# Kernel optimization log

Measured on AMD Instinct MI355X. Metric: run time of the kernel, lower is better.

The kernel has to match this reference:

```python
import jax, jax.numpy as jnp
import numpy as np

N_EDGE_TYPES = 25
EF = 2  # edge feature dim (excluding type)
HID = 10


def _edge_nn(et, ef, emb, wh, bh, wg, bg):
    # y = relu(emb[et] * (ef@Wh+bh) + (ef@Wg+bg)) -> [E, in*out]
    return jax.nn.relu(emb[et] * (ef @ wh + bh) + (ef @ wg + bg))


def _nnconv(x, et, ef, src, dst, emb, wh, bh, wg, bg, root, bias, in_c, out_c):
    n = x.shape[0]
    w = _edge_nn(et, ef, emb, wh, bh, wg, bg).reshape(-1, in_c, out_c)  # [E,in,out]
    msg = jnp.einsum('ei,eio->eo', x[src], w)                          # per-edge matmul
    s = jax.ops.segment_sum(msg, dst, num_segments=n)
    cnt = jax.ops.segment_sum(jnp.ones((src.shape[0],), x.dtype), dst, num_segments=n)
    agg = s / jnp.maximum(cnt, 1.0)[:, None]                           # scatter-mean
    return agg + x @ root + bias


def _make_params(key, in_c, out_c):
    ks = jax.random.split(key, 6)
    d = in_c * out_c
    s = 0.1
    return dict(
        emb=jax.random.normal(ks[0], (N_EDGE_TYPES, d), jnp.float32) * s,
        wh=jax.random.normal(ks[1], (EF, d), jnp.float32) * s,
        bh=jax.random.normal(ks[2], (d,), jnp.float32) * s,
        wg=jax.random.normal(ks[3], (EF, d), jnp.float32) * s,
        bg=jax.random.normal(ks[4], (d,), jnp.float32) * s,
        root=jax.random.normal(ks[5], (in_c, out_c), jnp.float32) * s,
        bias=jnp.zeros((out_c,), jnp.float32),
    )


def setup_inputs() -> dict:
    key = jax.random.key(0)
    ks = jax.random.split(key, 12)
    N, E, IN_C, OUT_C, B = 50000, 250000, 16, 16, 8
    inp = {
        'x': jax.random.normal(ks[0], (N, IN_C), jnp.float32),
        'edge_feat': jax.random.normal(ks[1], (E, EF), jnp.float32),
        'edge_type': jax.random.randint(ks[2], (E,), 0, N_EDGE_TYPES),
        'edge_src': jax.random.randint(ks[3], (E,), 0, N),
        'edge_dst': jax.random.randint(ks[4], (E,), 0, N),
        'cell_type': jax.random.randint(ks[5], (N,), 0, 3),
        'batch_ids': jnp.sort(jax.random.randint(ks[6], (N,), 0, B)),
        'batch_size': B,
    }
    for i, (ic, oc) in enumerate([(IN_C, HID), (HID, HID), (HID, OUT_C)], start=1):
        p = _make_params(ks[6 + i], ic, oc)
        for k, v in p.items():
            inp[f'{k}{i}'] = v
    return inp


def reference(x, edge_feat,
              emb1, wh1, bh1, wg1, bg1, root1, bias1,
              emb2, wh2, bh2, wg2, bg2, root2, bias2,
              emb3, wh3, bh3, wg3, bg3, root3, bias3,
              edge_type, edge_src, edge_dst, cell_type, batch_ids, batch_size):
    in_c, out_c = x.shape[1], root3.shape[1]
    h = _nnconv(x, edge_type, edge_feat, edge_src, edge_dst,
                emb1, wh1, bh1, wg1, bg1, root1, bias1, in_c, HID)
    h = jax.nn.relu(h)  # dropout is identity in eval mode
    h = _nnconv(h, edge_type, edge_feat, edge_src, edge_dst,
                emb2, wh2, bh2, wg2, bg2, root2, bias2, HID, HID)
    h = jax.nn.relu(h)
    h = _nnconv(h, edge_type, edge_feat, edge_src, edge_dst,
                emb3, wh3, bh3, wg3, bg3, root3, bias3, HID, out_c)
    h = jax.nn.relu(h)
    # scatter-mean pooling over nodes with cell_type==1, grouped by graph id
    gate = (cell_type == 1).astype(jnp.int32)
    idx = gate * (batch_ids.astype(jnp.int32) + 1)  # 0 = discarded bucket
    nseg = batch_size + 1
    s = jax.ops.segment_sum(h, idx, num_segments=nseg)
    cnt = jax.ops.segment_sum(jnp.ones((h.shape[0],), h.dtype), idx, num_segments=nseg)
    pooled = s / jnp.maximum(cnt, 1.0)[:, None]
    return pooled[1:batch_size + 1, :]  # [B, out_c]
```

## Files before the change

### kernel.cpp

```cpp
#include <hip/hip_runtime.h>
#include <stdint.h>

#define IN1 16
#define HIDC 10
#define OUT3 16
#define NTYPES 25
#define MAXB 8
#define HSTR 12

#define D1 (IN1 * HIDC)
#define D2 (HIDC * HIDC)
#define D3 (HIDC * OUT3)

__global__ __launch_bounds__(256) void init_kernel(
    const float* __restrict__ emb1, const float* __restrict__ wh1,
    const float* __restrict__ bh1, const float* __restrict__ wg1,
    const float* __restrict__ bg1,
    const float* __restrict__ emb2, const float* __restrict__ wh2,
    const float* __restrict__ bh2, const float* __restrict__ wg2,
    const float* __restrict__ bg2,
    const float* __restrict__ emb3, const float* __restrict__ wh3,
    const float* __restrict__ bh3, const float* __restrict__ wg3,
    const float* __restrict__ bg3,
    float4* __restrict__ P1, float4* __restrict__ P2, float4* __restrict__ P3,
    int* __restrict__ deg, int N,
    float* __restrict__ psum, float* __restrict__ pcnt, int B)
{
  int gtid = blockIdx.x * 256 + threadIdx.x;
  int gstr = gridDim.x * 256;
  const int nPrep = NTYPES * (D1 + D2 + D3);
  for (int i = gtid; i < nPrep; i += gstr) {
    const float *emb, *wh, *bh, *wg, *bg; float4* P; int D, k;
    if (i < NTYPES * D1) {
      emb = emb1; wh = wh1; bh = bh1; wg = wg1; bg = bg1; P = P1; D = D1; k = i;
    } else if (i < NTYPES * (D1 + D2)) {
      emb = emb2; wh = wh2; bh = bh2; wg = wg2; bg = bg2; P = P2; D = D2;
      k = i - NTYPES * D1;
    } else {
      emb = emb3; wh = wh3; bh = bh3; wg = wg3; bg = bg3; P = P3; D = D3;
      k = i - NTYPES * (D1 + D2);
    }
    int j = k - (k / D) * D;
    float e = emb[k];
    float4 p;
    p.x = fmaf(e, wh[j],     wg[j]);
    p.y = fmaf(e, wh[D + j], wg[D + j]);
    p.z = fmaf(e, bh[j],     bg[j]);
    p.w = 0.f;
    P[k] = p;
  }
  for (int i = gtid; i < N; i += gstr) deg[i] = 0;
  for (int i = gtid; i < B * 16; i += gstr) psum[i] = 0.f;
  for (int i = gtid; i < B; i += gstr) pcnt[i] = 0.f;
}

__global__ __launch_bounds__(256) void hist_kernel(const int* __restrict__ edst,
                                                   int* __restrict__ deg,
                                                   int* __restrict__ pos, int E) {
  int e = blockIdx.x * blockDim.x + threadIdx.x;
  if (e < E) pos[e] = atomicAdd(&deg[edst[e]], 1);
}

__global__ __launch_bounds__(256) void scan_part_kernel(const int* __restrict__ deg,
                                                        int* __restrict__ row_ptr,
                                                        int* __restrict__ bsum, int N) {
  __shared__ int wsums[4];
  int tid = threadIdx.x, lane = tid & 63, wid = tid >> 6;
  int idx0 = (blockIdx.x * 256 + tid) * 4;
  int4 v = make_int4(0, 0, 0, 0);
  if (idx0 < N)     v.x = deg[idx0];
  if (idx0 + 1 < N) v.y = deg[idx0 + 1];
  if (idx0 + 2 < N) v.z = deg[idx0 + 2];
  if (idx0 + 3 < N) v.w = deg[idx0 + 3];
  int s = v.x + v.y + v.z + v.w;
  int x = s;
  #pragma unroll
  for (int off = 1; off < 64; off <<= 1) {
    int y = __shfl_up(x, off);
    if (lane >= off) x += y;
  }
  if (lane == 63) wsums[wid] = x;
  __syncthreads();
  int wpre = 0;
  #pragma unroll
  for (int w = 0; w < 4; ++w) if (w < wid) wpre += wsums[w];
  int excl = x - s + wpre;
  if (idx0 < N)     row_ptr[idx0]     = excl;
  if (idx0 + 1 < N) row_ptr[idx0 + 1] = excl + v.x;
  if (idx0 + 2 < N) row_ptr[idx0 + 2] = excl + v.x + v.y;
  if (idx0 + 3 < N) row_ptr[idx0 + 3] = excl + v.x + v.y + v.z;
  if (tid == 255) bsum[blockIdx.x] = excl + s;
}

__global__ __launch_bounds__(256) void scan_add2_kernel(int* __restrict__ row_ptr,
                                                        const int* __restrict__ bsum,
                                                        int N, int chunks) {
  __shared__ int s_off;
  int c = blockIdx.x, tid = threadIdx.x;
  if (tid < 64) {
    int v = (tid < c) ? bsum[tid] : 0;
    #pragma unroll
    for (int off = 32; off >= 1; off >>= 1) v += __shfl_xor(v, off);
    if (tid == 0) s_off = v;
  }
  __syncthreads();
  int off = s_off;
  int base = c * 1024 + tid * 4;
  #pragma unroll
  for (int j = 0; j < 4; ++j) {
    int idx = base + j;
    if (idx < N) row_ptr[idx] += off;
  }
  if (c == chunks - 1 && tid == 0) row_ptr[N] = off + bsum[c];
}

__global__ __launch_bounds__(256) void permute_kernel(
    const int* __restrict__ edst, const int* __restrict__ esrc,
    const int* __restrict__ et, const float2* __restrict__ ef,
    const int* __restrict__ row_ptr, const int* __restrict__ pos,
    int4* __restrict__ edges, int E) {
  int e = blockIdx.x * blockDim.x + threadIdx.x;
  if (e >= E) return;
  int d = edst[e];
  int idx = row_ptr[d] + pos[e];
  float2 f = ef[e];
  int4 r;
  r.x = esrc[e];
  r.y = et[e];
  r.z = __float_as_int(f.x);
  r.w = __float_as_int(f.y);
  edges[idx] = r;
}

template<int IN_C, int O, int XS, bool POOL, int BS>
__global__ __launch_bounds__(BS) void layer_kernel(
    const float* __restrict__ xin, const int4* __restrict__ edges,
    const int* __restrict__ row_ptr, const float4* __restrict__ Pg,
    const float* __restrict__ root, const float* __restrict__ bias,
    float* __restrict__ hout, const int* __restrict__ ctype,
    const int* __restrict__ bids, float* __restrict__ pcnt, int N, int B)
{
  constexpr int D = IN_C * O;
  constexpr int TSTR = D + 1;
  constexpr int NPB = BS / 16;
  __shared__ float4 s_P[NTYPES * TSTR];
  __shared__ float s_psum[POOL ? (MAXB * 16) : 1];
  __shared__ float s_pcnt[POOL ? MAXB : 1];

  int tid = threadIdx.x;
  for (int k = tid; k < NTYPES * D; k += BS) {
    int t = k / D, j = k - t * D;
    s_P[t * TSTR + j] = Pg[k];
  }
  if (POOL) {
    for (int i = tid; i < MAXB * 16; i += BS) s_psum[i] = 0.f;
    for (int i = tid; i < MAXB; i += BS) s_pcnt[i] = 0.f;
  }
  __syncthreads();

  int nl = tid >> 4;
  int o = tid & 15;
  int oc = (O == 16) ? o : ((o < O) ? o : 0);
  int n = blockIdx.x * NPB + nl;

  float acc = 0.f;
  int start = 0, end = 0;
  if (n < N) { start = row_ptr[n]; end = row_ptr[n + 1]; }
  for (int e = start; e < end; ++e) {
    int4 r = edges[e];
    float f0 = __int_as_float(r.z), f1 = __int_as_float(r.w);
    const float4* __restrict__ pb = s_P + r.y * TSTR + oc;
    const float* __restrict__ xr = xin + (size_t)r.x * XS;
    #pragma unroll
    for (int q = 0; q < IN_C / 4; ++q) {
      float4 xq = ((const float4*)xr)[q];
      float4 p0 = pb[(4 * q + 0) * O];
      float4 p1 = pb[(4 * q + 1) * O];
      float4 p2 = pb[(4 * q + 2) * O];
      float4 p3 = pb[(4 * q + 3) * O];
      acc = fmaf(xq.x, fmaxf(fmaf(f0, p0.x, fmaf(f1, p0.y, p0.z)), 0.f), acc);
      acc = fmaf(xq.y, fmaxf(fmaf(f0, p1.x, fmaf(f1, p1.y, p1.z)), 0.f), acc);
      acc = fmaf(xq.z, fmaxf(fmaf(f0, p2.x, fmaf(f1, p2.y, p2.z)), 0.f), acc);
      acc = fmaf(xq.w, fmaxf(fmaf(f0, p3.x, fmaf(f1, p3.y, p3.z)), 0.f), acc);
    }
    if constexpr (IN_C % 4 == 2) {
      float2 xq = ((const float2*)xr)[IN_C / 2 - 1];
      float4 p0 = pb[(IN_C - 2) * O];
      float4 p1 = pb[(IN_C - 1) * O];
      acc = fmaf(xq.x, fmaxf(fmaf(f0, p0.x, fmaf(f1, p0.y, p0.z)), 0.f), acc);
      acc = fmaf(xq.y, fmaxf(fmaf(f0, p1.x, fmaf(f1, p1.y, p1.z)), 0.f), acc);
    }
  }

  if (n < N && o < O) {
    float inv = 1.0f / fmaxf((float)(end - start), 1.0f);
    float v = fmaf(acc, inv, bias[o]);
    const float* __restrict__ xr = xin + (size_t)n * XS;
    #pragma unroll
    for (int i = 0; i < IN_C; ++i) v = fmaf(xr[i], root[i * O + o], v);
    v = fmaxf(v, 0.f);
    if (!POOL) {
      hout[(size_t)n * HSTR + o] = v;
    } else {
      if (ctype[n] == 1) {
        int b = bids[n];
        atomicAdd(&s_psum[b * 16 + o], v);
        if (o == 0) atomicAdd(&s_pcnt[b], 1.0f);
      }
    }
  }

  if (POOL) {
    __syncthreads();
    for (int i = tid; i < B * 16; i += BS) {
      float v = s_psum[i];
      if (v != 0.f) atomicAdd(&hout[i], v);
    }
    for (int i = tid; i < B; i += BS) {
      float c = s_pcnt[i];
      if (c != 0.f) atomicAdd(&pcnt[i], c);
    }
  }
}

__global__ __launch_bounds__(256) void finalize_kernel(
    const float* __restrict__ psum, const float* __restrict__ pcnt,
    float* __restrict__ out, int B) {
  int i = blockIdx.x * blockDim.x + threadIdx.x;
  if (i >= B * OUT3) return;
  int b = i / OUT3;
  out[i] = psum[i] / fmaxf(pcnt[b], 1.0f);
}

extern "C" void kernel_launch(void* const* d_in, const int* in_sizes, int n_in,
                              void* d_out, int out_size, void* d_ws, size_t ws_size,
                              hipStream_t stream)
{
  const float* x     = (const float*)d_in[0];
  const float* ef    = (const float*)d_in[1];
  const int*   et    = (const int*)d_in[2];
  const int*   esrc  = (const int*)d_in[3];
  const int*   edst  = (const int*)d_in[4];
  const int*   ctype = (const int*)d_in[5];
  const int*   bids  = (const int*)d_in[6];
  const float* emb1 = (const float*)d_in[8];
  const float* wh1  = (const float*)d_in[9];
  const float* bh1  = (const float*)d_in[10];
  const float* wg1  = (const float*)d_in[11];
  const float* bg1  = (const float*)d_in[12];
  const float* root1= (const float*)d_in[13];
  const float* bias1= (const float*)d_in[14];
  const float* emb2 = (const float*)d_in[15];
  const float* wh2  = (const float*)d_in[16];
  const float* bh2  = (const float*)d_in[17];
  const float* wg2  = (const float*)d_in[18];
  const float* bg2  = (const float*)d_in[19];
  const float* root2= (const float*)d_in[20];
  const float* bias2= (const float*)d_in[21];
  const float* emb3 = (const float*)d_in[22];
  const float* wh3  = (const float*)d_in[23];
  const float* bh3  = (const float*)d_in[24];
  const float* wg3  = (const float*)d_in[25];
  const float* bg3  = (const float*)d_in[26];
  const float* root3= (const float*)d_in[27];
  const float* bias3= (const float*)d_in[28];

  const int N = in_sizes[0] / IN1;
  const int E = in_sizes[2];
  const int B = out_size / OUT3;

  int4* edges   = (int4*)d_ws;
  int*  deg     = (int*)(edges + E);
  int*  pos     = deg + N;
  int*  row_ptr = pos + E;
  int*  bsum    = row_ptr + (N + 1);
  uintptr_t pp  = ((uintptr_t)(bsum + 64) + 15) & ~(uintptr_t)15;
  float4* P1    = (float4*)pp;
  float4* P2    = P1 + NTYPES * D1;
  float4* P3    = P2 + NTYPES * D2;
  float* h1     = (float*)(P3 + NTYPES * D3);
  float* h2     = h1 + (size_t)N * HSTR;
  float* psum   = h2 + (size_t)N * HSTR;
  float* pcnt   = psum + (size_t)B * 16;

  const int nChunk = (N + 1023) / 1024;

  init_kernel<<<128, 256, 0, stream>>>(
      emb1, wh1, bh1, wg1, bg1, emb2, wh2, bh2, wg2, bg2,
      emb3, wh3, bh3, wg3, bg3, P1, P2, P3, deg, N, psum, pcnt, B);
  hist_kernel<<<(E + 255) / 256, 256, 0, stream>>>(edst, deg, pos, E);
  scan_part_kernel<<<nChunk, 256, 0, stream>>>(deg, row_ptr, bsum, N);
  scan_add2_kernel<<<nChunk, 256, 0, stream>>>(row_ptr, bsum, N, nChunk);
  permute_kernel<<<(E + 255) / 256, 256, 0, stream>>>(
      edst, esrc, et, (const float2*)ef, row_ptr, pos, edges, E);

  const int g512 = (N + 31) / 32;
  layer_kernel<IN1, HIDC, IN1, false, 512><<<g512, 512, 0, stream>>>(
      x, edges, row_ptr, P1, root1, bias1,
      h1, nullptr, nullptr, nullptr, N, B);
  layer_kernel<HIDC, HIDC, HSTR, false, 512><<<g512, 512, 0, stream>>>(
      h1, edges, row_ptr, P2, root2, bias2,
      h2, nullptr, nullptr, nullptr, N, B);

  const int g1024 = (N + 63) / 64;
  layer_kernel<HIDC, OUT3, HSTR, true, 1024><<<g1024, 1024, 0, stream>>>(
      h2, edges, row_ptr, P3, root3, bias3,
      psum, ctype, bids, pcnt, N, B);

  finalize_kernel<<<1, 256, 0, stream>>>(psum, pcnt, (float*)d_out, B);
}
```

Before: 254.0 us.

## Sort nodes by in-degree into buckets to balance per-wave edge loops

```diff
diff --git a/kernel.cpp b/kernel.cpp
--- a/kernel.cpp
+++ b/kernel.cpp
@@ -6,6 +6,7 @@
 #define OUT3 16
 #define NTYPES 25
 #define MAXB 8
+#define NBUCK 32
 #define HSTR 12
 
 #define D1 (IN1 * HIDC)
@@ -24,7 +25,8 @@
     const float* __restrict__ bg3,
     float4* __restrict__ P1, float4* __restrict__ P2, float4* __restrict__ P3,
     int* __restrict__ deg, int N,
-    float* __restrict__ psum, float* __restrict__ pcnt, int B)
+    float* __restrict__ psum, float* __restrict__ pcnt,
+    int* __restrict__ bcnt, int B)
 {
   int gtid = blockIdx.x * 256 + threadIdx.x;
   int gstr = gridDim.x * 256;
@@ -52,6 +54,7 @@
   for (int i = gtid; i < N; i += gstr) deg[i] = 0;
   for (int i = gtid; i < B * 16; i += gstr) psum[i] = 0.f;
   for (int i = gtid; i < B; i += gstr) pcnt[i] = 0.f;
+  if (gtid < NBUCK) bcnt[gtid] = 0;
 }
 
 __global__ __launch_bounds__(256) void hist_kernel(const int* __restrict__ edst,
@@ -63,15 +66,23 @@
 
 __global__ __launch_bounds__(256) void scan_part_kernel(const int* __restrict__ deg,
                                                         int* __restrict__ row_ptr,
-                                                        int* __restrict__ bsum, int N) {
+                                                        int* __restrict__ bsum,
+                                                        int* __restrict__ bcnt, int N) {
   __shared__ int wsums[4];
+  __shared__ int s_cnt[NBUCK];
   int tid = threadIdx.x, lane = tid & 63, wid = tid >> 6;
+  if (tid < NBUCK) s_cnt[tid] = 0;
   int idx0 = (blockIdx.x * 256 + tid) * 4;
   int4 v = make_int4(0, 0, 0, 0);
   if (idx0 < N)     v.x = deg[idx0];
   if (idx0 + 1 < N) v.y = deg[idx0 + 1];
   if (idx0 + 2 < N) v.z = deg[idx0 + 2];
   if (idx0 + 3 < N) v.w = deg[idx0 + 3];
+  __syncthreads();
+  if (idx0 < N)     atomicAdd(&s_cnt[min(v.x, NBUCK - 1)], 1);
+  if (idx0 + 1 < N) atomicAdd(&s_cnt[min(v.y, NBUCK - 1)], 1);
+  if (idx0 + 2 < N) atomicAdd(&s_cnt[min(v.z, NBUCK - 1)], 1);
+  if (idx0 + 3 < N) atomicAdd(&s_cnt[min(v.w, NBUCK - 1)], 1);
   int s = v.x + v.y + v.z + v.w;
   int x = s;
   #pragma unroll
@@ -90,10 +101,14 @@
   if (idx0 + 2 < N) row_ptr[idx0 + 2] = excl + v.x + v.y;
   if (idx0 + 3 < N) row_ptr[idx0 + 3] = excl + v.x + v.y + v.z;
   if (tid == 255) bsum[blockIdx.x] = excl + s;
+  __syncthreads();
+  if (tid < NBUCK && s_cnt[tid] > 0) atomicAdd(&bcnt[tid], s_cnt[tid]);
 }
 
 __global__ __launch_bounds__(256) void scan_add2_kernel(int* __restrict__ row_ptr,
                                                         const int* __restrict__ bsum,
+                                                        const int* __restrict__ bcnt,
+                                                        int* __restrict__ boff,
                                                         int N, int chunks) {
   __shared__ int s_off;
   int c = blockIdx.x, tid = threadIdx.x;
@@ -103,6 +118,17 @@
     for (int off = 32; off >= 1; off >>= 1) v += __shfl_xor(v, off);
     if (tid == 0) s_off = v;
   }
+  if (c == 0 && tid >= 64 && tid < 128) {
+    int l = tid - 64;
+    int b = (l < NBUCK) ? bcnt[l] : 0;
+    int x = b;
+    #pragma unroll
+    for (int off = 1; off < NBUCK; off <<= 1) {
+      int y = __shfl_up(x, off);
+      if (l >= off) x += y;
+    }
+    if (l < NBUCK) boff[l] = x - b;
+  }
   __syncthreads();
   int off = s_off;
   int base = c * 1024 + tid * 4;
@@ -112,6 +138,26 @@
     if (idx < N) row_ptr[idx] += off;
   }
   if (c == chunks - 1 && tid == 0) row_ptr[N] = off + bsum[c];
+}
+
+__global__ __launch_bounds__(256) void assign_kernel(const int* __restrict__ deg,
+                                                     int* __restrict__ boff,
+                                                     int* __restrict__ order, int N) {
+  __shared__ int s_cnt[NBUCK];
+  __shared__ int s_base[NBUCK];
+  int tid = threadIdx.x;
+  if (tid < NBUCK) s_cnt[tid] = 0;
+  __syncthreads();
+  int n = blockIdx.x * 256 + tid;
+  int b = 0, lr = 0;
+  if (n < N) {
+    b = min(deg[n], NBUCK - 1);
+    lr = atomicAdd(&s_cnt[b], 1);
+  }
+  __syncthreads();
+  if (tid < NBUCK && s_cnt[tid] > 0) s_base[tid] = atomicAdd(&boff[tid], s_cnt[tid]);
+  __syncthreads();
+  if (n < N) order[s_base[b] + lr] = n;
 }
 
 __global__ __launch_bounds__(256) void permute_kernel(
@@ -135,7 +181,8 @@
 template<int IN_C, int O, int XS, bool POOL, int BS>
 __global__ __launch_bounds__(BS) void layer_kernel(
     const float* __restrict__ xin, const int4* __restrict__ edges,
-    const int* __restrict__ row_ptr, const float4* __restrict__ Pg,
+    const int* __restrict__ row_ptr, const int* __restrict__ order,
+    const float4* __restrict__ Pg,
     const float* __restrict__ root, const float* __restrict__ bias,
     float* __restrict__ hout, const int* __restrict__ ctype,
     const int* __restrict__ bids, float* __restrict__ pcnt, int N, int B)
@@ -161,7 +208,8 @@
   int nl = tid >> 4;
   int o = tid & 15;
   int oc = (O == 16) ? o : ((o < O) ? o : 0);
-  int n = blockIdx.x * NPB + nl;
+  int idx = blockIdx.x * NPB + nl;
+  int n = (idx < N) ? order[idx] : N;
 
   float acc = 0.f;
   int start = 0, end = 0;
@@ -274,7 +322,10 @@
   int*  pos     = deg + N;
   int*  row_ptr = pos + E;
   int*  bsum    = row_ptr + (N + 1);
-  uintptr_t pp  = ((uintptr_t)(bsum + 64) + 15) & ~(uintptr_t)15;
+  int*  bcnt    = bsum + 64;
+  int*  boff    = bcnt + NBUCK;
+  int*  order   = boff + NBUCK;
+  uintptr_t pp  = ((uintptr_t)(order + N) + 15) & ~(uintptr_t)15;
   float4* P1    = (float4*)pp;
   float4* P2    = P1 + NTYPES * D1;
   float4* P3    = P2 + NTYPES * D2;
@@ -287,24 +338,25 @@
 
   init_kernel<<<128, 256, 0, stream>>>(
       emb1, wh1, bh1, wg1, bg1, emb2, wh2, bh2, wg2, bg2,
-      emb3, wh3, bh3, wg3, bg3, P1, P2, P3, deg, N, psum, pcnt, B);
+      emb3, wh3, bh3, wg3, bg3, P1, P2, P3, deg, N, psum, pcnt, bcnt, B);
   hist_kernel<<<(E + 255) / 256, 256, 0, stream>>>(edst, deg, pos, E);
-  scan_part_kernel<<<nChunk, 256, 0, stream>>>(deg, row_ptr, bsum, N);
-  scan_add2_kernel<<<nChunk, 256, 0, stream>>>(row_ptr, bsum, N, nChunk);
+  scan_part_kernel<<<nChunk, 256, 0, stream>>>(deg, row_ptr, bsum, bcnt, N);
+  scan_add2_kernel<<<nChunk, 256, 0, stream>>>(row_ptr, bsum, bcnt, boff, N, nChunk);
+  assign_kernel<<<(N + 255) / 256, 256, 0, stream>>>(deg, boff, order, N);
   permute_kernel<<<(E + 255) / 256, 256, 0, stream>>>(
       edst, esrc, et, (const float2*)ef, row_ptr, pos, edges, E);
 
   const int g512 = (N + 31) / 32;
   layer_kernel<IN1, HIDC, IN1, false, 512><<<g512, 512, 0, stream>>>(
-      x, edges, row_ptr, P1, root1, bias1,
+      x, edges, row_ptr, order, P1, root1, bias1,
       h1, nullptr, nullptr, nullptr, N, B);
   layer_kernel<HIDC, HIDC, HSTR, false, 512><<<g512, 512, 0, stream>>>(
-      h1, edges, row_ptr, P2, root2, bias2,
+      h1, edges, row_ptr, order, P2, root2, bias2,
       h2, nullptr, nullptr, nullptr, N, B);
 
   const int g1024 = (N + 63) / 64;
   layer_kernel<HIDC, OUT3, HSTR, true, 1024><<<g1024, 1024, 0, stream>>>(
-      h2, edges, row_ptr, P3, root3, bias3,
+      h2, edges, row_ptr, order, P3, root3, bias3,
       psum, ctype, bids, pcnt, N, B);
 
   finalize_kernel<<<1, 256, 0, stream>>>(psum, pcnt, (float*)d_out, B);
```

New measurement: 255.2 us. Within noise of the previous version (+0.5%).
